# Performance work log

Measured on AMD Instinct MI355X. Metric: run time of the kernel, lower is better.

## Reference

```python
import jax, jax.numpy as jnp
import numpy as np

EPS = 1e-12  # torch F.normalize eps


def _l2_normalize(x):
    norm = jnp.sqrt(jnp.sum(x * x, axis=-1, keepdims=True))
    return x / jnp.maximum(norm, EPS)


def setup_inputs() -> dict:
    key = jax.random.key(0)
    k1, k2 = jax.random.split(key)
    b, seq, hid = 64, 2048, 256
    r_s = jax.random.normal(k1, (b, seq, hid), dtype=jnp.float32)
    r_t = jax.random.normal(k2, (b, seq, hid), dtype=jnp.float32)
    return {"r_s": r_s, "r_t": r_t}


def reference(r_s, r_t):
    # r_s, r_t: [b, seq, hid]
    b = r_s.shape[0]
    K = b - 1
    rs = _l2_normalize(r_s)
    rt = _l2_normalize(r_t)

    # Pairwise cosine similarity at matching seq positions: sim[i, j, s] = <rs[i,s], rt[j,s]>
    sim = jnp.einsum('ish,jsh->ijs', rs, rt)          # [b, b, seq]
    sim_ii = jnp.einsum('ish,ish->is', rs, rt)        # diagonal, [b, seq]

    pos_score = 1.0 - sim_ii                          # [b, seq]
    # sum over j != i of (2 - (g_neg - g_pos)) where g(x,y) = 1 - <x,y>
    #   = sum_{j!=i} (2 - sim_ii + sim_ij)
    sim_sum_offdiag = jnp.sum(sim, axis=1) - sim_ii   # [b, seq]
    neg_sum = K * (2.0 - sim_ii) + sim_sum_offdiag    # [b, seq]
    neg_score = neg_sum / (2.0 * K)

    loss = jnp.sum(pos_score + neg_score) / (b * 200 * (K + 1) * 4)
    return loss
```

## Files before the change

kernel.cpp:

```cpp
#include <hip/hip_runtime.h>
#include <math.h>

#define BATCH 64
#define SEQ   2048
#define HID   256
#define KNEG  63

#define INV_DENOM (1.0f / 3276800.0f)

__global__ __launch_bounds__(256) void cosnce_per_s(
    const float* __restrict__ rs, const float* __restrict__ rt,
    float* __restrict__ partial) {
  const int s    = blockIdx.x;
  const int tid  = threadIdx.x;
  const int wave = tid >> 6;
  const int lane = tid & 63;

  __shared__ float S_sh[4][HID];
  __shared__ float T_sh[4][HID];
  __shared__ float D_sh[4];
  __shared__ float red_sh[4];

  float S0 = 0.f, S1 = 0.f, S2 = 0.f, S3 = 0.f;
  float T0 = 0.f, T1 = 0.f, T2 = 0.f, T3 = 0.f;
  float D  = 0.f;

  const size_t col = (size_t)lane * 4;

#pragma unroll 4
  for (int ii = 0; ii < 16; ++ii) {
    const int i = wave * 16 + ii;
    const size_t base = ((size_t)i * SEQ + s) * HID + col;
    const float4 a = *(const float4*)(rs + base);
    const float4 b = *(const float4*)(rt + base);

    float ss = a.x * a.x + a.y * a.y + a.z * a.z + a.w * a.w;
    float tt = b.x * b.x + b.y * b.y + b.z * b.z + b.w * b.w;
    float st = a.x * b.x + a.y * b.y + a.z * b.z + a.w * b.w;

#pragma unroll
    for (int off = 32; off > 0; off >>= 1) {
      ss += __shfl_xor(ss, off);
      tt += __shfl_xor(tt, off);
      st += __shfl_xor(st, off);
    }

    const float inv_s = 1.f / fmaxf(sqrtf(ss), 1e-12f);
    const float inv_t = 1.f / fmaxf(sqrtf(tt), 1e-12f);

    D  += st * inv_s * inv_t;
    S0 += a.x * inv_s; S1 += a.y * inv_s; S2 += a.z * inv_s; S3 += a.w * inv_s;
    T0 += b.x * inv_t; T1 += b.y * inv_t; T2 += b.z * inv_t; T3 += b.w * inv_t;
  }

  *(float4*)&S_sh[wave][col] = make_float4(S0, S1, S2, S3);
  *(float4*)&T_sh[wave][col] = make_float4(T0, T1, T2, T3);
  if (lane == 0) D_sh[wave] = D;
  __syncthreads();

  float Ssum = S_sh[0][tid] + S_sh[1][tid] + S_sh[2][tid] + S_sh[3][tid];
  float Tsum = T_sh[0][tid] + T_sh[1][tid] + T_sh[2][tid] + T_sh[3][tid];
  float prod = Ssum * Tsum;
#pragma unroll
  for (int off = 32; off > 0; off >>= 1) prod += __shfl_xor(prod, off);
  if (lane == 0) red_sh[wave] = prod;
  __syncthreads();

  if (tid == 0) {
    const float STdot = red_sh[0] + red_sh[1] + red_sh[2] + red_sh[3];
    const float Dtot  = D_sh[0] + D_sh[1] + D_sh[2] + D_sh[3];
    const float inv2K = 1.f / (2.f * (float)KNEG);
    const float c = 2.f * (float)BATCH - (1.5f + inv2K) * Dtot + STdot * inv2K;
    partial[s] = c * INV_DENOM;
  }
}

__global__ __launch_bounds__(256) void cosnce_reduce(
    const float* __restrict__ partial, float* __restrict__ out) {
  const int tid  = threadIdx.x;
  const int wave = tid >> 6;
  const int lane = tid & 63;
  float acc = 0.f;
  for (int idx = tid; idx < SEQ; idx += 256) acc += partial[idx];
#pragma unroll
  for (int off = 32; off > 0; off >>= 1) acc += __shfl_xor(acc, off);
  __shared__ float sh[4];
  if (lane == 0) sh[wave] = acc;
  __syncthreads();
  if (tid == 0) out[0] = sh[0] + sh[1] + sh[2] + sh[3];
}

extern "C" void kernel_launch(void* const* d_in, const int* in_sizes, int n_in,
                              void* d_out, int out_size, void* d_ws, size_t ws_size,
                              hipStream_t stream) {
  const float* rs = (const float*)d_in[0];
  const float* rt = (const float*)d_in[1];
  float* out      = (float*)d_out;
  float* partial  = (float*)d_ws;

  cosnce_per_s<<<SEQ, 256, 0, stream>>>(rs, rt, partial);
  cosnce_reduce<<<1, 256, 0, stream>>>(partial, out);
}
```

Measured before the change: 52.45 us.

## Fuse final reduction via last-block atomic counter and regroup lanes for shorter shuffles

The two-kernel scheme becomes one: each block writes its partial and bumps an atomic counter, and the last block to finish sums all partials. Each wave now splits into 4 groups of 16 lanes, so one wave processes four rows at once with 16-lane shuffle reductions and reads more data per lane. The normalization uses a hardware rsq on the clamped squared norm. This adds a memset launch and extra cross-lane shuffles for the accumulators, and it relies on the fence and atomic ordering being correct.

New measurement: 115.8 us. 121% more time.

```diff
diff --git a/kernel.cpp b/kernel.cpp
--- a/kernel.cpp
+++ b/kernel.cpp
@@ -8,54 +8,105 @@
 
 #define INV_DENOM (1.0f / 3276800.0f)
 
-__global__ __launch_bounds__(256) void cosnce_per_s(
+__device__ __forceinline__ float dot4(const float4& u, const float4& v) {
+  return u.x * v.x + u.y * v.y + u.z * v.z + u.w * v.w;
+}
+__device__ __forceinline__ void fma4(float4& acc, const float4& v, float s) {
+  acc.x = fmaf(v.x, s, acc.x);
+  acc.y = fmaf(v.y, s, acc.y);
+  acc.z = fmaf(v.z, s, acc.z);
+  acc.w = fmaf(v.w, s, acc.w);
+}
+
+__global__ __launch_bounds__(256) void cosnce_fused(
     const float* __restrict__ rs, const float* __restrict__ rt,
-    float* __restrict__ partial) {
+    float* __restrict__ partial, unsigned int* __restrict__ counter,
+    float* __restrict__ out) {
   const int s    = blockIdx.x;
   const int tid  = threadIdx.x;
   const int wave = tid >> 6;
   const int lane = tid & 63;
+  const int g    = lane >> 4;
+  const int k    = lane & 15;
+
+  float4 Sacc0 = make_float4(0.f, 0.f, 0.f, 0.f), Sacc1 = Sacc0, Sacc2 = Sacc0, Sacc3 = Sacc0;
+  float4 Tacc0 = Sacc0, Tacc1 = Sacc0, Tacc2 = Sacc0, Tacc3 = Sacc0;
+  float  Dacc  = 0.f;
+
+#pragma unroll
+  for (int r = 0; r < 4; ++r) {
+    const int    i    = wave * 16 + r * 4 + g;
+    const size_t base = ((size_t)i * SEQ + s) * HID + k * 4;
+    const float* pa   = rs + base;
+    const float* pb   = rt + base;
+    const float4 a0 = *(const float4*)(pa);
+    const float4 a1 = *(const float4*)(pa + 64);
+    const float4 a2 = *(const float4*)(pa + 128);
+    const float4 a3 = *(const float4*)(pa + 192);
+    const float4 b0 = *(const float4*)(pb);
+    const float4 b1 = *(const float4*)(pb + 64);
+    const float4 b2 = *(const float4*)(pb + 128);
+    const float4 b3 = *(const float4*)(pb + 192);
+
+    float ss = dot4(a0, a0) + dot4(a1, a1) + dot4(a2, a2) + dot4(a3, a3);
+    float tt = dot4(b0, b0) + dot4(b1, b1) + dot4(b2, b2) + dot4(b3, b3);
+    float st = dot4(a0, b0) + dot4(a1, b1) + dot4(a2, b2) + dot4(a3, b3);
+
+#pragma unroll
+    for (int off = 1; off <= 8; off <<= 1) {
+      ss += __shfl_xor(ss, off);
+      tt += __shfl_xor(tt, off);
+      st += __shfl_xor(st, off);
+    }
+
+    const float inv_s = __builtin_amdgcn_rsqf(fmaxf(ss, 1e-24f));
+    const float inv_t = __builtin_amdgcn_rsqf(fmaxf(tt, 1e-24f));
+
+    Dacc = fmaf(st, inv_s * inv_t, Dacc);
+    fma4(Sacc0, a0, inv_s); fma4(Sacc1, a1, inv_s);
+    fma4(Sacc2, a2, inv_s); fma4(Sacc3, a3, inv_s);
+    fma4(Tacc0, b0, inv_t); fma4(Tacc1, b1, inv_t);
+    fma4(Tacc2, b2, inv_t); fma4(Tacc3, b3, inv_t);
+  }
+
+#pragma unroll
+  for (int off = 16; off <= 32; off <<= 1) {
+    Sacc0.x += __shfl_xor(Sacc0.x, off); Sacc0.y += __shfl_xor(Sacc0.y, off);
+    Sacc0.z += __shfl_xor(Sacc0.z, off); Sacc0.w += __shfl_xor(Sacc0.w, off);
+    Sacc1.x += __shfl_xor(Sacc1.x, off); Sacc1.y += __shfl_xor(Sacc1.y, off);
+    Sacc1.z += __shfl_xor(Sacc1.z, off); Sacc1.w += __shfl_xor(Sacc1.w, off);
+    Sacc2.x += __shfl_xor(Sacc2.x, off); Sacc2.y += __shfl_xor(Sacc2.y, off);
+    Sacc2.z += __shfl_xor(Sacc2.z, off); Sacc2.w += __shfl_xor(Sacc2.w, off);
+    Sacc3.x += __shfl_xor(Sacc3.x, off); Sacc3.y += __shfl_xor(Sacc3.y, off);
+    Sacc3.z += __shfl_xor(Sacc3.z, off); Sacc3.w += __shfl_xor(Sacc3.w, off);
+    Tacc0.x += __shfl_xor(Tacc0.x, off); Tacc0.y += __shfl_xor(Tacc0.y, off);
+    Tacc0.z += __shfl_xor(Tacc0.z, off); Tacc0.w += __shfl_xor(Tacc0.w, off);
+    Tacc1.x += __shfl_xor(Tacc1.x, off); Tacc1.y += __shfl_xor(Tacc1.y, off);
+    Tacc1.z += __shfl_xor(Tacc1.z, off); Tacc1.w += __shfl_xor(Tacc1.w, off);
+    Tacc2.x += __shfl_xor(Tacc2.x, off); Tacc2.y += __shfl_xor(Tacc2.y, off);
+    Tacc2.z += __shfl_xor(Tacc2.z, off); Tacc2.w += __shfl_xor(Tacc2.w, off);
+    Tacc3.x += __shfl_xor(Tacc3.x, off); Tacc3.y += __shfl_xor(Tacc3.y, off);
+    Tacc3.z += __shfl_xor(Tacc3.z, off); Tacc3.w += __shfl_xor(Tacc3.w, off);
+    Dacc += __shfl_xor(Dacc, off);
+  }
 
   __shared__ float S_sh[4][HID];
   __shared__ float T_sh[4][HID];
   __shared__ float D_sh[4];
   __shared__ float red_sh[4];
+  __shared__ unsigned int done_sh;
 
-  float S0 = 0.f, S1 = 0.f, S2 = 0.f, S3 = 0.f;
-  float T0 = 0.f, T1 = 0.f, T2 = 0.f, T3 = 0.f;
-  float D  = 0.f;
-
-  const size_t col = (size_t)lane * 4;
-
-#pragma unroll 4
-  for (int ii = 0; ii < 16; ++ii) {
-    const int i = wave * 16 + ii;
-    const size_t base = ((size_t)i * SEQ + s) * HID + col;
-    const float4 a = *(const float4*)(rs + base);
-    const float4 b = *(const float4*)(rt + base);
-
-    float ss = a.x * a.x + a.y * a.y + a.z * a.z + a.w * a.w;
-    float tt = b.x * b.x + b.y * b.y + b.z * b.z + b.w * b.w;
-    float st = a.x * b.x + a.y * b.y + a.z * b.z + a.w * b.w;
-
-#pragma unroll
-    for (int off = 32; off > 0; off >>= 1) {
-      ss += __shfl_xor(ss, off);
-      tt += __shfl_xor(tt, off);
-      st += __shfl_xor(st, off);
-    }
-
-    const float inv_s = 1.f / fmaxf(sqrtf(ss), 1e-12f);
-    const float inv_t = 1.f / fmaxf(sqrtf(tt), 1e-12f);
-
-    D  += st * inv_s * inv_t;
-    S0 += a.x * inv_s; S1 += a.y * inv_s; S2 += a.z * inv_s; S3 += a.w * inv_s;
-    T0 += b.x * inv_t; T1 += b.y * inv_t; T2 += b.z * inv_t; T3 += b.w * inv_t;
+  if (g == 0) {
+    *(float4*)&S_sh[wave][0 * 64 + k * 4] = Sacc0;
+    *(float4*)&S_sh[wave][1 * 64 + k * 4] = Sacc1;
+    *(float4*)&S_sh[wave][2 * 64 + k * 4] = Sacc2;
+    *(float4*)&S_sh[wave][3 * 64 + k * 4] = Sacc3;
+    *(float4*)&T_sh[wave][0 * 64 + k * 4] = Tacc0;
+    *(float4*)&T_sh[wave][1 * 64 + k * 4] = Tacc1;
+    *(float4*)&T_sh[wave][2 * 64 + k * 4] = Tacc2;
+    *(float4*)&T_sh[wave][3 * 64 + k * 4] = Tacc3;
+    if (k == 0) D_sh[wave] = Dacc;
   }
-
-  *(float4*)&S_sh[wave][col] = make_float4(S0, S1, S2, S3);
-  *(float4*)&T_sh[wave][col] = make_float4(T0, T1, T2, T3);
-  if (lane == 0) D_sh[wave] = D;
   __syncthreads();
 
   float Ssum = S_sh[0][tid] + S_sh[1][tid] + S_sh[2][tid] + S_sh[3][tid];
@@ -70,24 +121,23 @@
     const float STdot = red_sh[0] + red_sh[1] + red_sh[2] + red_sh[3];
     const float Dtot  = D_sh[0] + D_sh[1] + D_sh[2] + D_sh[3];
     const float inv2K = 1.f / (2.f * (float)KNEG);
-    const float c = 2.f * (float)BATCH - (1.5f + inv2K) * Dtot + STdot * inv2K;
-    partial[s] = c * INV_DENOM;
+    const float cres  = 2.f * (float)BATCH - (1.5f + inv2K) * Dtot + STdot * inv2K;
+    partial[s] = cres * INV_DENOM;
+    __threadfence();
+    done_sh = atomicAdd(counter, 1u);
   }
-}
+  __syncthreads();
 
-__global__ __launch_bounds__(256) void cosnce_reduce(
-    const float* __restrict__ partial, float* __restrict__ out) {
-  const int tid  = threadIdx.x;
-  const int wave = tid >> 6;
-  const int lane = tid & 63;
-  float acc = 0.f;
-  for (int idx = tid; idx < SEQ; idx += 256) acc += partial[idx];
+  if (done_sh == SEQ - 1) {
+    __threadfence();
+    float acc = 0.f;
+    for (int idx = tid; idx < SEQ; idx += 256) acc += partial[idx];
 #pragma unroll
-  for (int off = 32; off > 0; off >>= 1) acc += __shfl_xor(acc, off);
-  __shared__ float sh[4];
-  if (lane == 0) sh[wave] = acc;
-  __syncthreads();
-  if (tid == 0) out[0] = sh[0] + sh[1] + sh[2] + sh[3];
+    for (int off = 32; off > 0; off >>= 1) acc += __shfl_xor(acc, off);
+    if (lane == 0) red_sh[wave] = acc;
+    __syncthreads();
+    if (tid == 0) out[0] = red_sh[0] + red_sh[1] + red_sh[2] + red_sh[3];
+  }
 }
 
 extern "C" void kernel_launch(void* const* d_in, const int* in_sizes, int n_in,
@@ -97,7 +147,8 @@
   const float* rt = (const float*)d_in[1];
   float* out      = (float*)d_out;
   float* partial  = (float*)d_ws;
+  unsigned int* counter = (unsigned int*)((char*)d_ws + SEQ * sizeof(float));
 
-  cosnce_per_s<<<SEQ, 256, 0, stream>>>(rs, rt, partial);
-  cosnce_reduce<<<1, 256, 0, stream>>>(partial, out);
+  hipMemsetAsync(counter, 0, sizeof(unsigned int), stream);
+  cosnce_fused<<<SEQ, 256, 0, stream>>>(rs, rt, partial, counter, out);
 }
```

## Process four sequence positions per block with 512 threads and rsqrt

Applied to the files above, without the earlier changes.

Each block now handles four consecutive sequence positions using eight waves, so every batch row read becomes a contiguous 4 KB span and each thread keeps more independent loads in flight. The shuffle reductions are interleaved across the four positions, and the normalisation uses the hardware reciprocal square root. This cuts the block count by four and raises shared memory and register use per block, which may lower occupancy.

Result: slower. 62.18 us (+18.6%).

```diff
diff --git a/kernel.cpp b/kernel.cpp
--- a/kernel.cpp
+++ b/kernel.cpp
@@ -5,73 +5,115 @@
 #define SEQ   2048
 #define HID   256
 #define KNEG  63
+#define SGRP  4
 
 #define INV_DENOM (1.0f / 3276800.0f)
 
-__global__ __launch_bounds__(256) void cosnce_per_s(
+__device__ __forceinline__ float dot4(const float4& u, const float4& v) {
+  return u.x * v.x + u.y * v.y + u.z * v.z + u.w * v.w;
+}
+__device__ __forceinline__ void fma4(float4& acc, const float4& v, float s) {
+  acc.x = fmaf(v.x, s, acc.x);
+  acc.y = fmaf(v.y, s, acc.y);
+  acc.z = fmaf(v.z, s, acc.z);
+  acc.w = fmaf(v.w, s, acc.w);
+}
+
+__global__ __launch_bounds__(512, 4) void cosnce_per_s(
     const float* __restrict__ rs, const float* __restrict__ rt,
     float* __restrict__ partial) {
-  const int s    = blockIdx.x;
+  const int s0   = blockIdx.x * SGRP;
   const int tid  = threadIdx.x;
   const int wave = tid >> 6;
   const int lane = tid & 63;
+  const int col  = lane * 4;
 
-  __shared__ float S_sh[4][HID];
-  __shared__ float T_sh[4][HID];
-  __shared__ float D_sh[4];
-  __shared__ float red_sh[4];
+  float4 Sacc[SGRP], Tacc[SGRP];
+  float  Dacc[SGRP];
+#pragma unroll
+  for (int k = 0; k < SGRP; ++k) {
+    Sacc[k] = make_float4(0.f, 0.f, 0.f, 0.f);
+    Tacc[k] = Sacc[k];
+    Dacc[k] = 0.f;
+  }
 
-  float S0 = 0.f, S1 = 0.f, S2 = 0.f, S3 = 0.f;
-  float T0 = 0.f, T1 = 0.f, T2 = 0.f, T3 = 0.f;
-  float D  = 0.f;
+#pragma unroll 2
+  for (int r = 0; r < 8; ++r) {
+    const int    i  = wave * 8 + r;
+    const size_t bo = ((size_t)i * SEQ + s0) * HID + col;
+    const float* pa = rs + bo;
+    const float* pb = rt + bo;
 
-  const size_t col = (size_t)lane * 4;
+    float4 a[SGRP], b[SGRP];
+#pragma unroll
+    for (int k = 0; k < SGRP; ++k) a[k] = *(const float4*)(pa + k * HID);
+#pragma unroll
+    for (int k = 0; k < SGRP; ++k) b[k] = *(const float4*)(pb + k * HID);
 
-#pragma unroll 4
-  for (int ii = 0; ii < 16; ++ii) {
-    const int i = wave * 16 + ii;
-    const size_t base = ((size_t)i * SEQ + s) * HID + col;
-    const float4 a = *(const float4*)(rs + base);
-    const float4 b = *(const float4*)(rt + base);
-
-    float ss = a.x * a.x + a.y * a.y + a.z * a.z + a.w * a.w;
-    float tt = b.x * b.x + b.y * b.y + b.z * b.z + b.w * b.w;
-    float st = a.x * b.x + a.y * b.y + a.z * b.z + a.w * b.w;
+    float ss[SGRP], tt[SGRP], st[SGRP];
+#pragma unroll
+    for (int k = 0; k < SGRP; ++k) {
+      ss[k] = dot4(a[k], a[k]);
+      tt[k] = dot4(b[k], b[k]);
+      st[k] = dot4(a[k], b[k]);
+    }
 
 #pragma unroll
-    for (int off = 32; off > 0; off >>= 1) {
-      ss += __shfl_xor(ss, off);
-      tt += __shfl_xor(tt, off);
-      st += __shfl_xor(st, off);
+    for (int off = 1; off <= 32; off <<= 1) {
+#pragma unroll
+      for (int k = 0; k < SGRP; ++k) {
+        ss[k] += __shfl_xor(ss[k], off);
+        tt[k] += __shfl_xor(tt[k], off);
+        st[k] += __shfl_xor(st[k], off);
+      }
     }
 
-    const float inv_s = 1.f / fmaxf(sqrtf(ss), 1e-12f);
-    const float inv_t = 1.f / fmaxf(sqrtf(tt), 1e-12f);
-
-    D  += st * inv_s * inv_t;
-    S0 += a.x * inv_s; S1 += a.y * inv_s; S2 += a.z * inv_s; S3 += a.w * inv_s;
-    T0 += b.x * inv_t; T1 += b.y * inv_t; T2 += b.z * inv_t; T3 += b.w * inv_t;
+#pragma unroll
+    for (int k = 0; k < SGRP; ++k) {
+      const float inv_s = __builtin_amdgcn_rsqf(fmaxf(ss[k], 1e-24f));
+      const float inv_t = __builtin_amdgcn_rsqf(fmaxf(tt[k], 1e-24f));
+      Dacc[k] = fmaf(st[k], inv_s * inv_t, Dacc[k]);
+      fma4(Sacc[k], a[k], inv_s);
+      fma4(Tacc[k], b[k], inv_t);
+    }
   }
 
-  *(float4*)&S_sh[wave][col] = make_float4(S0, S1, S2, S3);
-  *(float4*)&T_sh[wave][col] = make_float4(T0, T1, T2, T3);
-  if (lane == 0) D_sh[wave] = D;
+  __shared__ float S_sh[8][SGRP][HID];
+  __shared__ float T_sh[8][SGRP][HID];
+  __shared__ float D_sh[8][SGRP];
+
+#pragma unroll
+  for (int k = 0; k < SGRP; ++k) {
+    *(float4*)&S_sh[wave][k][col] = Sacc[k];
+    *(float4*)&T_sh[wave][k][col] = Tacc[k];
+  }
+  if (lane == 0) {
+#pragma unroll
+    for (int k = 0; k < SGRP; ++k) D_sh[wave][k] = Dacc[k];
+  }
   __syncthreads();
 
-  float Ssum = S_sh[0][tid] + S_sh[1][tid] + S_sh[2][tid] + S_sh[3][tid];
-  float Tsum = T_sh[0][tid] + T_sh[1][tid] + T_sh[2][tid] + T_sh[3][tid];
-  float prod = Ssum * Tsum;
+  if (wave < SGRP) {
+    const int k = wave;
+    float4 Ssum = make_float4(0.f, 0.f, 0.f, 0.f), Tsum = Ssum;
 #pragma unroll
-  for (int off = 32; off > 0; off >>= 1) prod += __shfl_xor(prod, off);
-  if (lane == 0) red_sh[wave] = prod;
-  __syncthreads();
-
-  if (tid == 0) {
-    const float STdot = red_sh[0] + red_sh[1] + red_sh[2] + red_sh[3];
-    const float Dtot  = D_sh[0] + D_sh[1] + D_sh[2] + D_sh[3];
-    const float inv2K = 1.f / (2.f * (float)KNEG);
-    const float c = 2.f * (float)BATCH - (1.5f + inv2K) * Dtot + STdot * inv2K;
-    partial[s] = c * INV_DENOM;
+    for (int w = 0; w < 8; ++w) {
+      const float4 sv = *(const float4*)&S_sh[w][k][col];
+      const float4 tv = *(const float4*)&T_sh[w][k][col];
+      Ssum.x += sv.x; Ssum.y += sv.y; Ssum.z += sv.z; Ssum.w += sv.w;
+      Tsum.x += tv.x; Tsum.y += tv.y; Tsum.z += tv.z; Tsum.w += tv.w;
+    }
+    float prod = dot4(Ssum, Tsum);
+#pragma unroll
+    for (int off = 1; off <= 32; off <<= 1) prod += __shfl_xor(prod, off);
+    if (lane == 0) {
+      float Dtot = 0.f;
+#pragma unroll
+      for (int w = 0; w < 8; ++w) Dtot += D_sh[w][k];
+      const float inv2K = 1.f / (2.f * (float)KNEG);
+      const float cres  = 2.f * (float)BATCH - (1.5f + inv2K) * Dtot + prod * inv2K;
+      partial[s0 + k] = cres * INV_DENOM;
+    }
   }
 }
 
@@ -98,6 +140,6 @@
   float* out      = (float*)d_out;
   float* partial  = (float*)d_ws;
 
-  cosnce_per_s<<<SEQ, 256, 0, stream>>>(rs, rt, partial);
+  cosnce_per_s<<<SEQ / SGRP, 512, 0, stream>>>(rs, rt, partial);
   cosnce_reduce<<<1, 256, 0, stream>>>(partial, out);
 }
```
